# Optimization experiments

Hardware: AMD Instinct MI355X
Metric: run time of the kernel (lower is better)

## Reference

```python
import jax, jax.numpy as jnp
import numpy as np

TEMPERATURE = 0.1
NORMALIZED = True


def _l2norm(x, eps=1e-12):
    # matches F.normalize(p=2, dim=1)
    n = jnp.sqrt(jnp.sum(x * x, axis=1, keepdims=True))
    return x / jnp.maximum(n, eps)


def setup_inputs() -> dict:
    key = jax.random.key(0)
    k1, k2, k3, k4 = jax.random.split(key, 4)
    B, D = 4096, 256
    return {
        "hs": jax.random.normal(k1, (B, D), dtype=jnp.float32),
        "ht0": jax.random.normal(k2, (B, D), dtype=jnp.float32),
        "ht1": jax.random.normal(k3, (B, D), dtype=jnp.float32),
        "labels": jax.random.randint(k4, (B,), 0, 100, dtype=jnp.int64)
        if jax.config.jax_enable_x64 else jax.random.randint(k4, (B,), 0, 100, dtype=jnp.int32),
        "num_views": 2,
    }


def _per_teacher_loss(hs_n, ht_n, mask, logits_mask, batch_size, num_views):
    # features: [N, D] with N = 2B
    features = jnp.concatenate([hs_n, ht_n], axis=0)
    sim = jnp.matmul(features, features.T) / TEMPERATURE          # [N, N]
    exp_logits = jnp.exp(sim) * logits_mask                        # [N, N]
    log_prob = sim - jnp.log(jnp.sum(exp_logits, axis=1, keepdims=True))
    per_inst = -jnp.sum(mask * log_prob, axis=1) / jnp.sum(mask, axis=1)  # [N]
    if num_views > 1:
        per_inst = per_inst.reshape(batch_size, num_views).mean(axis=1)
    return per_inst.mean()


def reference(hs, ht0, ht1, labels, num_views):
    batch_size = labels.shape[0]
    hs = hs.reshape(batch_size, -1)
    ht_list = [ht0.reshape(batch_size, -1), ht1.reshape(batch_size, -1)]
    if NORMALIZED:
        hs = _l2norm(hs)
        ht_list = [_l2norm(ht) for ht in ht_list]

    labels2 = jnp.concatenate([labels, labels])                    # [N]
    mask = (labels2[:, None] == labels2[None, :]).astype(jnp.float32)
    N = 2 * batch_size
    logits_mask = 1.0 - jnp.eye(N, dtype=jnp.float32)              # zero diagonal
    mask = mask * logits_mask

    inter_loss = 0.0
    for ht in ht_list:
        inter_loss = inter_loss + _per_teacher_loss(
            hs, ht, mask, logits_mask, batch_size, num_views)
    return inter_loss / len(ht_list)
```

## Files before the change

### kernel.cpp

```cpp
#include <hip/hip_runtime.h>
#include <hip/hip_bf16.h>

#define B_SIZE 4096
#define D_SIZE 256
#define N_SIZE 8192
#define LOG2E10 14.4269504089f

#if __has_builtin(__builtin_amdgcn_exp2f)
#define FAST_EXP2(x) __builtin_amdgcn_exp2f(x)
#else
#define FAST_EXP2(x) __expf((x) * 0.69314718056f)
#endif

typedef __attribute__((ext_vector_type(8))) short short8;
typedef __attribute__((ext_vector_type(4))) short short4v;
typedef __attribute__((ext_vector_type(4))) float floatx4;


__device__ __forceinline__ void async16(void* lds, const void* g) {
    __builtin_amdgcn_global_load_lds(
        (const __attribute__((address_space(1))) unsigned int*)g,
        (__attribute__((address_space(3))) unsigned int*)lds, 16, 0, 0);
}

__global__ void norm_kernel(const float* __restrict__ hs,
                            const float* __restrict__ ht0,
                            const float* __restrict__ ht1,
                            __hip_bfloat16* __restrict__ dst,
                            float* __restrict__ zero_region,
                            const int* __restrict__ labels,
                            int* __restrict__ cnt, int* __restrict__ offv,
                            int* __restrict__ idxS) {
    const int tid = threadIdx.x;
    const int wv  = tid >> 6;
    const int l   = tid & 63;
    const int gid = blockIdx.x * 256 + tid;
    if (gid < 16386) zero_region[gid] = 0.0f;

    const int row = blockIdx.x * 4 + wv;
    const float* src = (row < 4096) ? (hs + row * D_SIZE)
                     : (row < 8192) ? (ht0 + (row - 4096) * D_SIZE)
                                    : (ht1 + (row - 8192) * D_SIZE);
    floatx4 x = *reinterpret_cast<const floatx4*>(src + l * 4);
    float ss = x[0] * x[0] + x[1] * x[1] + x[2] * x[2] + x[3] * x[3];
#pragma unroll
    for (int off = 32; off > 0; off >>= 1) ss += __shfl_xor(ss, off);
    float inv = 1.0f / fmaxf(sqrtf(ss), 1e-12f);
    short4v o;
#pragma unroll
    for (int k = 0; k < 4; ++k) {
        __hip_bfloat16 h = __float2bfloat16(x[k] * inv);
        o[k] = *reinterpret_cast<short*>(&h);
    }
    *reinterpret_cast<short4v*>(dst + row * D_SIZE + l * 4) = o;

    if (blockIdx.x == 0) {
        __shared__ int h[128], o2[128], ctr[128];
        if (tid < 128) { h[tid] = 0; ctr[tid] = 0; }
        __syncthreads();
        for (int i = tid; i < B_SIZE; i += 256) atomicAdd(&h[labels[i] & 127], 1);
        __syncthreads();
        if (tid == 0) {
            int s = 0;
            for (int c = 0; c < 128; ++c) { o2[c] = s; s += h[c]; }
        }
        __syncthreads();
        for (int i = tid; i < B_SIZE; i += 256) {
            int lab = labels[i] & 127;
            int pos = o2[lab] + atomicAdd(&ctr[lab], 1);
            idxS[pos] = i;
        }
        if (tid < 128) { cnt[tid] = h[tid]; offv[tid] = o2[tid]; }
    }
}

__global__ void gvec_kernel(const __hip_bfloat16* __restrict__ featBase,
                            const int* __restrict__ cnt,
                            const int* __restrict__ off,
                            const int* __restrict__ idxS,
                            float* __restrict__ gOut) {
    const int c   = blockIdx.x & 127;
    const int set = blockIdx.x >> 7;
    const int tid = threadIdx.x;
    const __hip_bfloat16* f = featBase + set * B_SIZE * D_SIZE;
    __shared__ int sIdx[256];
    const int n = cnt[c], o = off[c];
    float acc = 0.0f;
    for (int base = 0; base < n; base += 256) {
        int m = n - base; if (m > 256) m = 256;
        __syncthreads();
        if (tid < m) sIdx[tid] = idxS[o + base + tid];
        __syncthreads();
        for (int k = 0; k < m; ++k)
            acc += __bfloat162float(f[sIdx[k] * D_SIZE + tid]);
    }
    gOut[set * 32768 + c * 256 + tid] = acc;
}

__global__ __launch_bounds__(512, 2)
void sim_kernel(const __hip_bfloat16* __restrict__ featS,
                const __hip_bfloat16* __restrict__ featT0,
                const __hip_bfloat16* __restrict__ featT1,
                float* __restrict__ Sarr) {
    __shared__ __align__(16) unsigned char sB[4][32768];

    const int tid  = threadIdx.x;
    const int w    = tid >> 6;
    const int l    = tid & 63;
    const int quad = l >> 4;
    const int lcol = l & 15;

    int RB, C, t;
    if (blockIdx.x < 480) {
        t = blockIdx.x & 1;
        int q = blockIdx.x >> 1;
        int r = (int)((1.0f + sqrtf(1.0f + 4.0f * (float)q)) * 0.5f);
        while (r * (r - 1) > q) --r;
        while (r * (r + 1) <= q) ++r;
        RB = r; C = q - r * (r - 1);
    } else {
        int i = blockIdx.x - 480;
        t = i & 1;
        int s = i >> 1;
        RB = s >> 1;
        C = (RB << 1) + (s & 1);
    }

    const __hip_bfloat16* featT = t ? featT1 : featT0;
    const int row_base = RB * 512 + w * 64;
    const int col0 = C * 256;

    short8 af[4][8];
#pragma unroll
    for (int rt = 0; rt < 4; ++rt) {
        int arow = row_base + rt * 16 + lcol;
        const __hip_bfloat16* ap = (arow < B_SIZE) ? featS + arow * D_SIZE
                                                   : featT + (arow - B_SIZE) * D_SIZE;
#pragma unroll
        for (int ks = 0; ks < 8; ++ks)
            af[rt][ks] = *reinterpret_cast<const short8*>(ap + ks * 32 + quad * 8);
    }

    {
        const int u   = w >> 1;
        const int ks0 = (w & 1) * 4;
        const int tb  = col0 + u * 16;
        const __hip_bfloat16* cp = (tb < B_SIZE) ? featS + tb * D_SIZE
                                                 : featT + (tb - B_SIZE) * D_SIZE;
        const char* gp = (const char*)cp + (l & 15) * 512 + (l >> 4) * 16;
#pragma unroll
        for (int g = 0; g < 4; ++g)
#pragma unroll
            for (int kk = 0; kk < 4; ++kk) {
                int ks = ks0 + kk;
                async16(&sB[g][u * 8192 + ks * 1024], gp + g * 32768 + ks * 64);
            }
    }

    float Sp[4][4];
#pragma unroll
    for (int rt = 0; rt < 4; ++rt)
#pragma unroll
        for (int r = 0; r < 4; ++r) Sp[rt][r] = 0.0f;

    __syncthreads();

    for (int g = 0; g < 4; ++g) {
        const int gcol = col0 + g * 64;
        if (gcol > row_base) continue;
        const bool dg = (gcol == row_base);

        float Cp[4] = {0.f, 0.f, 0.f, 0.f};
#pragma unroll
        for (int up = 0; up < 2; ++up) {
            floatx4 acc[2][4];
#pragma unroll
            for (int j = 0; j < 2; ++j)
#pragma unroll
                for (int rt = 0; rt < 4; ++rt) acc[j][rt] = floatx4{0.f, 0.f, 0.f, 0.f};

#pragma unroll
            for (int ks = 0; ks < 8; ++ks) {
                short8 bf[2];
#pragma unroll
                for (int j = 0; j < 2; ++j)
                    bf[j] = *reinterpret_cast<const short8*>(
                        &sB[g][(up * 2 + j) * 8192 + ks * 1024 + l * 16]);
#pragma unroll
                for (int j = 0; j < 2; ++j)
#pragma unroll
                    for (int rt = 0; rt < 4; ++rt)
                        acc[j][rt] = __builtin_amdgcn_mfma_f32_16x16x32_bf16(
                            af[rt][ks], bf[j], acc[j][rt], 0, 0, 0);
            }
#pragma unroll
            for (int j = 0; j < 2; ++j)
#pragma unroll
                for (int rt = 0; rt < 4; ++rt)
#pragma unroll
                    for (int r = 0; r < 4; ++r) {
                        float e = FAST_EXP2(acc[j][rt][r] * LOG2E10);
                        Sp[rt][r] += e;
                        Cp[up * 2 + j] += e;
                    }
        }

        if (!dg) {
#pragma unroll
            for (int u = 0; u < 4; ++u) {
                Cp[u] += __shfl_xor(Cp[u], 16);
                Cp[u] += __shfl_xor(Cp[u], 32);
            }
            if (quad == 0) {
#pragma unroll
                for (int u = 0; u < 4; ++u)
                    atomicAdd(&Sarr[t * N_SIZE + gcol + u * 16 + lcol], Cp[u]);
            }
        }
    }

#pragma unroll
    for (int rt = 0; rt < 4; ++rt)
#pragma unroll
        for (int r = 0; r < 4; ++r) {
#pragma unroll
            for (int m = 1; m < 16; m <<= 1) Sp[rt][r] += __shfl_xor(Sp[rt][r], m);
        }
    if (lcol == 0) {
#pragma unroll
        for (int rt = 0; rt < 4; ++rt)
#pragma unroll
            for (int r = 0; r < 4; ++r) {
                int row = row_base + rt * 16 + quad * 4 + r;
                atomicAdd(&Sarr[t * N_SIZE + row], Sp[rt][r]);
            }
    }
}

__global__ void rowstat_kernel(const __hip_bfloat16* __restrict__ featS,
                               const __hip_bfloat16* __restrict__ featT0,
                               const __hip_bfloat16* __restrict__ featT1,
                               const int* __restrict__ labels,
                               const float* __restrict__ gAll,
                               const int* __restrict__ cnt,
                               const float* __restrict__ Sarr,
                               float* __restrict__ lossAcc,
                               int* __restrict__ ticket,
                               float* __restrict__ out) {
    __shared__ float wpart[4];
    const int tid = threadIdx.x;
    const int wv  = tid >> 6;
    const int l   = tid & 63;
    const int waveid = blockIdx.x * 4 + wv;
    float psum = 0.0f;

    for (int it = 0; it < 8; ++it) {
        int R = waveid * 8 + it;
        int t = R >> 13;
        int i = R & (N_SIZE - 1);
        const __hip_bfloat16* f = (i < B_SIZE) ? featS + i * D_SIZE
                                : (t ? featT1 : featT0) + (i - B_SIZE) * D_SIZE;
        int lab = labels[i & (B_SIZE - 1)] & 127;
        short4v fb = *reinterpret_cast<const short4v*>(f + l * 4);
        float fx[4];
#pragma unroll
        for (int k = 0; k < 4; ++k) {
            unsigned int u = ((unsigned int)(unsigned short)fb[k]) << 16;
            fx[k] = __uint_as_float(u);
        }
        const float* gS = gAll + lab * 256 + l * 4;
        const float* gT = gAll + (1 + t) * 32768 + lab * 256 + l * 4;
        float dot = 0.f, aii = 0.f;
#pragma unroll
        for (int k = 0; k < 4; ++k) {
            dot += fx[k] * (gS[k] + gT[k]);
            aii += fx[k] * fx[k];
        }
#pragma unroll
        for (int m = 1; m < 64; m <<= 1) {
            dot += __shfl_xor(dot, m);
            aii += __shfl_xor(aii, m);
        }
        if (l == 0) {
            float S = Sarr[t * N_SIZE + i];
            float M = 2.0f * (float)cnt[lab] - 1.0f;
            float E = FAST_EXP2(LOG2E10 * aii);
            psum += logf(S - E) - 10.0f * (dot - aii) / M;
        }
    }
    if (l == 0) wpart[wv] = psum;
    __syncthreads();
    if (tid == 0) {
        atomicAdd(lossAcc, wpart[0] + wpart[1] + wpart[2] + wpart[3]);
        __threadfence();
        if (atomicAdd(ticket, 1) == 511) {
            float tot = atomicAdd(lossAcc, 0.0f);
            out[0] = tot / 16384.0f;
        }
    }
}

extern "C" void kernel_launch(void* const* d_in, const int* in_sizes, int n_in,
                              void* d_out, int out_size, void* d_ws, size_t ws_size,
                              hipStream_t stream) {
    const float* hs     = (const float*)d_in[0];
    const float* ht0    = (const float*)d_in[1];
    const float* ht1    = (const float*)d_in[2];
    const int*   labels = (const int*)d_in[3];

    char* ws = (char*)d_ws;
    float* Sarr    = (float*)(ws);
    float* lossAcc = (float*)(ws + 65536);
    int*   ticket  = (int*)(ws + 65540);
    int*   cnt     = (int*)(ws + 66048);
    int*   offv    = (int*)(ws + 66560);
    int*   idxS    = (int*)(ws + 67072);
    float* gAll    = (float*)(ws + 83968);
    __hip_bfloat16* featS  = (__hip_bfloat16*)(ws + 524288);
    __hip_bfloat16* featT0 = (__hip_bfloat16*)(ws + 524288 + 2097152);
    __hip_bfloat16* featT1 = (__hip_bfloat16*)(ws + 524288 + 2 * 2097152);

    norm_kernel<<<3072, 256, 0, stream>>>(hs, ht0, ht1, featS, (float*)ws,
                                          labels, cnt, offv, idxS);
    gvec_kernel<<<384, 256, 0, stream>>>(featS, cnt, offv, idxS, gAll);
    sim_kernel<<<544, 512, 0, stream>>>(featS, featT0, featT1, Sarr);
    rowstat_kernel<<<512, 256, 0, stream>>>(featS, featT0, featT1, labels, gAll, cnt,
                                            Sarr, lossAcc, ticket, (float*)d_out);
}
```

Measured before the change: 177.0 us.

## Rebalance sim kernel per-wave over triangular bands with double-buffered async B tiles

The sim kernel now assigns work per wave instead of per block. Each wave takes a 64-row band and a contiguous chunk of the lower-triangle column units, with the number of chunks growing along the band so waves get balanced work. Each wave streams its own 16-column B tiles into a private double-buffered LDS slot and uses vmcnt waits in place of block-wide barriers. This removes the idle waves that skipped above-diagonal groups and the shared staging sync. In exchange, B tiles are no longer shared across waves, so global/L2 traffic per MFMA goes up and each block has fewer threads.

```diff
diff --git a/kernel.cpp b/kernel.cpp
--- a/kernel.cpp
+++ b/kernel.cpp
@@ -11,6 +11,9 @@
 #else
 #define FAST_EXP2(x) __expf((x) * 0.69314718056f)
 #endif
+
+#define WAITCNT_VM8 0x0F78
+#define WAITCNT_VM0 0x0F70
 
 typedef __attribute__((ext_vector_type(8))) short short8;
 typedef __attribute__((ext_vector_type(4))) short short4v;
@@ -97,12 +100,12 @@
     gOut[set * 32768 + c * 256 + tid] = acc;
 }
 
-__global__ __launch_bounds__(512, 2)
+__global__ __launch_bounds__(256, 2)
 void sim_kernel(const __hip_bfloat16* __restrict__ featS,
                 const __hip_bfloat16* __restrict__ featT0,
                 const __hip_bfloat16* __restrict__ featT1,
                 float* __restrict__ Sarr) {
-    __shared__ __align__(16) unsigned char sB[4][32768];
+    __shared__ __align__(16) unsigned char sB[4][2][8192];
 
     const int tid  = threadIdx.x;
     const int w    = tid >> 6;
@@ -110,30 +113,28 @@
     const int quad = l >> 4;
     const int lcol = l & 15;
 
-    int RB, C, t;
-    if (blockIdx.x < 480) {
-        t = blockIdx.x & 1;
-        int q = blockIdx.x >> 1;
-        int r = (int)((1.0f + sqrtf(1.0f + 4.0f * (float)q)) * 0.5f);
-        while (r * (r - 1) > q) --r;
-        while (r * (r + 1) <= q) ++r;
-        RB = r; C = q - r * (r - 1);
-    } else {
-        int i = blockIdx.x - 480;
-        t = i & 1;
-        int s = i >> 1;
-        RB = s >> 1;
-        C = (RB << 1) + (s & 1);
-    }
+    const int W   = blockIdx.x * 4 + w;
+    const int t   = W >= 1088;
+    const int wid = W - t * 1088;
+
+    int k = 0;
+    while (4 * (k + 1) * (k + 2) <= wid) ++k;
+    const int rem   = wid - 4 * k * (k + 1);
+    const int band  = 8 * k + rem / (k + 1);
+    const int chunk = rem % (k + 1);
+    const int units = band + 1;
+    const int per   = (units + k) / (k + 1);
+    const int u0    = chunk * per;
+    const int u1    = (u0 + per < units) ? (u0 + per) : units;
+    const int ng    = (u1 - u0) * 4;
 
     const __hip_bfloat16* featT = t ? featT1 : featT0;
-    const int row_base = RB * 512 + w * 64;
-    const int col0 = C * 256;
+    const int row0 = band * 64;
 
     short8 af[4][8];
 #pragma unroll
     for (int rt = 0; rt < 4; ++rt) {
-        int arow = row_base + rt * 16 + lcol;
+        int arow = row0 + rt * 16 + lcol;
         const __hip_bfloat16* ap = (arow < B_SIZE) ? featS + arow * D_SIZE
                                                    : featT + (arow - B_SIZE) * D_SIZE;
 #pragma unroll
@@ -141,87 +142,70 @@
             af[rt][ks] = *reinterpret_cast<const short8*>(ap + ks * 32 + quad * 8);
     }
 
-    {
-        const int u   = w >> 1;
-        const int ks0 = (w & 1) * 4;
-        const int tb  = col0 + u * 16;
-        const __hip_bfloat16* cp = (tb < B_SIZE) ? featS + tb * D_SIZE
-                                                 : featT + (tb - B_SIZE) * D_SIZE;
+    auto stage = [&](int buf, int cb) {
+        const __hip_bfloat16* cp = (cb < B_SIZE) ? featS + cb * D_SIZE
+                                                 : featT + (cb - B_SIZE) * D_SIZE;
         const char* gp = (const char*)cp + (l & 15) * 512 + (l >> 4) * 16;
-#pragma unroll
-        for (int g = 0; g < 4; ++g)
-#pragma unroll
-            for (int kk = 0; kk < 4; ++kk) {
-                int ks = ks0 + kk;
-                async16(&sB[g][u * 8192 + ks * 1024], gp + g * 32768 + ks * 64);
+        unsigned char* lp = &sB[w][buf][0];
+#pragma unroll
+        for (int ks = 0; ks < 8; ++ks)
+            async16(lp + ks * 1024, gp + ks * 64);
+    };
+
+    float Sp[4][4];
+#pragma unroll
+    for (int rt = 0; rt < 4; ++rt)
+#pragma unroll
+        for (int r = 0; r < 4; ++r) Sp[rt][r] = 0.0f;
+
+    stage(0, u0 * 64);
+
+    for (int gi = 0; gi < ng; ++gi) {
+        const int unit = u0 + (gi >> 2);
+        const int cb   = unit * 64 + (gi & 3) * 16;
+        const int buf  = gi & 1;
+
+        if (gi + 1 < ng) {
+            const int unit2 = u0 + ((gi + 1) >> 2);
+            stage(buf ^ 1, unit2 * 64 + ((gi + 1) & 3) * 16);
+            __builtin_amdgcn_s_waitcnt(WAITCNT_VM8);
+        } else {
+            __builtin_amdgcn_s_waitcnt(WAITCNT_VM0);
+        }
+
+        floatx4 acc[4];
+#pragma unroll
+        for (int rt = 0; rt < 4; ++rt) acc[rt] = floatx4{0.f, 0.f, 0.f, 0.f};
+
+#pragma unroll
+        for (int ks = 0; ks < 8; ++ks) {
+            short8 bf = *reinterpret_cast<const short8*>(&sB[w][buf][ks * 1024 + l * 16]);
+#pragma unroll
+            for (int rt = 0; rt < 4; ++rt)
+                acc[rt] = __builtin_amdgcn_mfma_f32_16x16x32_bf16(af[rt][ks], bf, acc[rt], 0, 0, 0);
+        }
+
+        float csum = 0.0f;
+#pragma unroll
+        for (int rt = 0; rt < 4; ++rt)
+#pragma unroll
+            for (int r = 0; r < 4; ++r) {
+                float e = FAST_EXP2(acc[rt][r] * LOG2E10);
+                Sp[rt][r] += e;
+                csum += e;
             }
-    }
-
-    float Sp[4][4];
+
+        if (unit != band) {
+            csum += __shfl_xor(csum, 16);
+            csum += __shfl_xor(csum, 32);
+            if (quad == 0)
+                atomicAdd(&Sarr[t * N_SIZE + cb + lcol], csum);
+        }
+    }
+
 #pragma unroll
     for (int rt = 0; rt < 4; ++rt)
 #pragma unroll
-        for (int r = 0; r < 4; ++r) Sp[rt][r] = 0.0f;
-
-    __syncthreads();
-
-    for (int g = 0; g < 4; ++g) {
-        const int gcol = col0 + g * 64;
-        if (gcol > row_base) continue;
-        const bool dg = (gcol == row_base);
-
-        float Cp[4] = {0.f, 0.f, 0.f, 0.f};
-#pragma unroll
-        for (int up = 0; up < 2; ++up) {
-            floatx4 acc[2][4];
-#pragma unroll
-            for (int j = 0; j < 2; ++j)
-#pragma unroll
-                for (int rt = 0; rt < 4; ++rt) acc[j][rt] = floatx4{0.f, 0.f, 0.f, 0.f};
-
-#pragma unroll
-            for (int ks = 0; ks < 8; ++ks) {
-                short8 bf[2];
-#pragma unroll
-                for (int j = 0; j < 2; ++j)
-                    bf[j] = *reinterpret_cast<const short8*>(
-                        &sB[g][(up * 2 + j) * 8192 + ks * 1024 + l * 16]);
-#pragma unroll
-                for (int j = 0; j < 2; ++j)
-#pragma unroll
-                    for (int rt = 0; rt < 4; ++rt)
-                        acc[j][rt] = __builtin_amdgcn_mfma_f32_16x16x32_bf16(
-                            af[rt][ks], bf[j], acc[j][rt], 0, 0, 0);
-            }
-#pragma unroll
-            for (int j = 0; j < 2; ++j)
-#pragma unroll
-                for (int rt = 0; rt < 4; ++rt)
-#pragma unroll
-                    for (int r = 0; r < 4; ++r) {
-                        float e = FAST_EXP2(acc[j][rt][r] * LOG2E10);
-                        Sp[rt][r] += e;
-                        Cp[up * 2 + j] += e;
-                    }
-        }
-
-        if (!dg) {
-#pragma unroll
-            for (int u = 0; u < 4; ++u) {
-                Cp[u] += __shfl_xor(Cp[u], 16);
-                Cp[u] += __shfl_xor(Cp[u], 32);
-            }
-            if (quad == 0) {
-#pragma unroll
-                for (int u = 0; u < 4; ++u)
-                    atomicAdd(&Sarr[t * N_SIZE + gcol + u * 16 + lcol], Cp[u]);
-            }
-        }
-    }
-
-#pragma unroll
-    for (int rt = 0; rt < 4; ++rt)
-#pragma unroll
         for (int r = 0; r < 4; ++r) {
 #pragma unroll
             for (int m = 1; m < 16; m <<= 1) Sp[rt][r] += __shfl_xor(Sp[rt][r], m);
@@ -231,7 +215,7 @@
         for (int rt = 0; rt < 4; ++rt)
 #pragma unroll
             for (int r = 0; r < 4; ++r) {
-                int row = row_base + rt * 16 + quad * 4 + r;
+                int row = row0 + rt * 16 + quad * 4 + r;
                 atomicAdd(&Sarr[t * N_SIZE + row], Sp[rt][r]);
             }
     }
@@ -323,7 +307,7 @@
     norm_kernel<<<3072, 256, 0, stream>>>(hs, ht0, ht1, featS, (float*)ws,
                                           labels, cnt, offv, idxS);
     gvec_kernel<<<384, 256, 0, stream>>>(featS, cnt, offv, idxS, gAll);
-    sim_kernel<<<544, 512, 0, stream>>>(featS, featT0, featT1, Sarr);
+    sim_kernel<<<544, 256, 0, stream>>>(featS, featT0, featT1, Sarr);
     rowstat_kernel<<<512, 256, 0, stream>>>(featS, featT0, featT1, labels, gAll, cnt,
                                             Sarr, lossAcc, ticket, (float*)d_out);
 }
```

Measured after the change: 202.3 us. 1.14x slower.
